# Optimization experiments

Hardware: AMD Instinct MI355X
Metric: run time of the kernel (lower is better)

Reference implementation:

```python
import jax, jax.numpy as jnp
import numpy as np

B, W, M = 16, 32, 512
NH, HALF, K, H = 64, 32, 8, 8
LK = W // 2               # long-conv kernel size
LOUT = W - 2 * (LK - 1)   # = 2 (dilated valid conv output length)
NSP = 10                  # n_spatial (hardcoded in module)
GC1_IN = (1 + LOUT) * K   # 24


def setup_inputs() -> dict:
    key = jax.random.key(0)
    ks = jax.random.split(key, 23)
    def n(k, shp, s=0.1):
        return jax.random.normal(k, shp, jnp.float32) * s
    return dict(
        x=jax.random.normal(ks[0], (B, W, M), jnp.float32),
        adj=jax.random.uniform(ks[1], (M, M), jnp.float32) / M,  # row-normalized-ish dense adj
        Wih=n(ks[2], (NH, 1)), Whh=n(ks[3], (NH, NH)),
        bih=n(ks[4], (NH,)), bhh=n(ks[5], (NH,)),
        W1=n(ks[6], (HALF, NH)), W2=n(ks[7], (HALF, NH)), b1=n(ks[8], (HALF,)),
        V=n(ks[9], (HALF,)), bv=n(ks[10], (1,)),
        Wb=n(ks[11], (M, M)), wb=n(ks[12], (1,)),
        conv_w=n(ks[13], (K, 1, W)), conv_b=n(ks[14], (K,)),
        convl_w=n(ks[15], (K, 1, LK)), convl_b=n(ks[16], (K,)),
        gc1_w=n(ks[17], (GC1_IN, NH)), gc1_b=n(ks[18], (NH,)),
        gc2_w=n(ks[19], (NH, NSP)), gc2_b=n(ks[20], (NSP,)),
        out_w=n(ks[21], (H, NSP + NH)), out_b=n(ks[22], (H,)),
    )


def reference(x, adj, Wih, Whh, bih, bhh, W1, W2, b1, V, bv, Wb, wb,
              conv_w, conv_b, convl_w, convl_b, gc1_w, gc1_b, gc2_w, gc2_b,
              out_w, out_b):
    b = x.shape[0]
    # [b, w, m] -> per-node sequences [b*m, w]
    seq = jnp.transpose(x, (0, 2, 1)).reshape(b * M, W)

    # vanilla tanh RNN, input_size=1 (batched over all b*m series)
    inp = seq[:, :, None] * Wih[:, 0] + (bih + bhh)          # [b*m, w, nh]
    def step(h, it):
        return jnp.tanh(it + h @ Whh.T), None
    h0 = jnp.zeros((b * M, NH), x.dtype)
    last_hid, _ = jax.lax.scan(step, h0, jnp.swapaxes(inp, 0, 1))
    last_hid = last_hid.reshape(b, M, NH)                    # out_temporal

    # pairwise additive attention: a[b,i,j] = V . elu(W1 h_j + W2 h_i + b1) + bv
    e1 = last_hid @ W1.T                                     # [b, m, half] (j role)
    e2 = last_hid @ W2.T                                     # [b, m, half] (i role)
    a = jax.nn.elu(e2[:, :, None, :] + e1[:, None, :, :] + b1)  # [b,m,m,half]
    a_mx = a @ V + bv                                        # [b, m, m]
    # F.normalize(p=2, dim=1)
    norm = jnp.sqrt(jnp.sum(a_mx * a_mx, axis=1, keepdims=True))
    a_mx = a_mx / jnp.maximum(norm, 1e-12)

    # per-node short conv (kernel == window -> out len 1) as a single matmul
    r_short = seq @ conv_w[:, 0, :].T + conv_b               # [b*m, k]
    # per-node dilated long conv, batched over all b*m series
    r_long = jax.lax.conv_general_dilated(
        seq[:, None, :], convl_w, window_strides=(1,), padding='VALID',
        rhs_dilation=(2,), dimension_numbers=('NCW', 'OIW', 'NCW'))
    r_long = r_long + convl_b[None, :, None]                 # [b*m, k, LOUT]
    r = jnp.concatenate([r_short[:, :, None], r_long], axis=-1)  # [b*m, k, 1+LOUT]
    r = jax.nn.relu(r.reshape(b, M, GC1_IN))

    # gated mix of static normalized adj and learned attention adj
    c = jax.nn.sigmoid(a_mx @ Wb + wb)
    adj_mix = adj[None] * c + a_mx * (1.0 - c)               # [b, m, m]

    # two dense graph conv layers: relu(adj @ (h @ W) + b)
    h1 = jax.nn.relu(adj_mix @ (r @ gc1_w) + gc1_b)          # [b, m, nh]
    out_spatial = jax.nn.relu(adj_mix @ (h1 @ gc2_w) + gc2_b)  # [b, m, nsp]

    feat = jnp.concatenate([out_spatial, last_hid], axis=-1)  # [b, m, nsp+nh]
    out = feat @ out_w.T + out_b                              # [b, m, h]
    return jnp.transpose(out, (0, 2, 1))                      # [b, h, m]
```

## Files before the change

kernel.cpp:

```cpp
#include <hip/hip_runtime.h>
#include <hip/hip_bf16.h>


typedef __attribute__((ext_vector_type(8))) short bf16x8;
typedef __attribute__((ext_vector_type(4))) float f32x4;
#define MFMA16 __builtin_amdgcn_mfma_f32_16x16x32_bf16

__device__ __forceinline__ unsigned short f2bf(float f) {
    unsigned u = __float_as_uint(f);
    u += 0x7fff + ((u >> 16) & 1);
    return (unsigned short)(u >> 16);
}
__device__ __forceinline__ float bf2f(unsigned short h) {
    return __uint_as_float(((unsigned)h) << 16);
}
__device__ __forceinline__ float fast_tanh(float x) {
    float e = __expf(2.f * x);
    return 1.f - 2.f / (e + 1.f);
}

__global__ __launch_bounds__(256) void wbt_kernel(
    const float* __restrict__ Wb, unsigned short* __restrict__ WbT)
{
    __shared__ float tile[32][33];
    int k0 = blockIdx.y * 32, n0 = blockIdx.x * 32;
    int t = threadIdx.x;
    for (int u = t; u < 1024; u += 256) {
        int r = u >> 5, c = u & 31;
        tile[r][c] = Wb[(k0 + r) * 512 + n0 + c];
    }
    __syncthreads();
    for (int u = t; u < 1024; u += 256) {
        int r = u >> 5, c = u & 31;
        WbT[(n0 + r) * 512 + k0 + c] = f2bf(tile[c][r]);
    }
}

__global__ __launch_bounds__(64) void rnn_kernel(
    const float* __restrict__ x, const float* __restrict__ Wih,
    const float* __restrict__ Whh, const float* __restrict__ bih,
    const float* __restrict__ bhh, float* __restrict__ lhT)
{
    int lane = threadIdx.x;
    int l15 = lane & 15, quad = lane >> 4;
    int row0 = blockIdx.x * 16;
    int b = row0 >> 9, m0 = row0 & 511;

    bf16x8 afr[4][2];
#pragma unroll
    for (int mt = 0; mt < 4; ++mt)
#pragma unroll
        for (int hf = 0; hf < 2; ++hf) {
            const float* src = Whh + (16 * mt + l15) * 64 + 32 * hf + quad * 8;
            union { bf16x8 v; unsigned short u[8]; } tmp;
#pragma unroll
            for (int j = 0; j < 8; ++j) tmp.u[j] = f2bf(src[j]);
            afr[mt][hf] = tmp.v;
        }
    float wihv[4][4], bsv[4][4];
#pragma unroll
    for (int mt = 0; mt < 4; ++mt)
#pragma unroll
        for (int r = 0; r < 4; ++r) {
            int n = 16 * mt + quad * 4 + r;
            wihv[mt][r] = Wih[n];
            bsv[mt][r]  = bih[n] + bhh[n];
        }

    __shared__ float xs[32][16];
    __shared__ __align__(16) unsigned short hs[16][72];
    for (int u = lane; u < 512; u += 64) {
        int t = u >> 4, mm = u & 15;
        xs[t][mm] = x[(b * 32 + t) * 512 + m0 + mm];
    }
    for (int u = lane; u < 16 * 72; u += 64) ((unsigned short*)hs)[u] = 0;
    __syncthreads();

    for (int t = 0; t < 32; ++t) {
        bf16x8 b0 = *(bf16x8*)(&hs[l15][quad * 8]);
        bf16x8 b1 = *(bf16x8*)(&hs[l15][32 + quad * 8]);
        float xt = xs[t][l15];
        f32x4 acc[4];
#pragma unroll
        for (int mt = 0; mt < 4; ++mt) {
            f32x4 z = {0.f, 0.f, 0.f, 0.f};
            acc[mt] = MFMA16(afr[mt][0], b0, z, 0, 0, 0);
            acc[mt] = MFMA16(afr[mt][1], b1, acc[mt], 0, 0, 0);
        }
#pragma unroll
        for (int mt = 0; mt < 4; ++mt) {
            ushort4 hw;
            float th[4];
#pragma unroll
            for (int r = 0; r < 4; ++r) {
                float v = acc[mt][r] + xt * wihv[mt][r] + bsv[mt][r];
                th[r] = fast_tanh(v);
            }
            hw.x = f2bf(th[0]); hw.y = f2bf(th[1]);
            hw.z = f2bf(th[2]); hw.w = f2bf(th[3]);
            *(ushort4*)(&hs[l15][16 * mt + quad * 4]) = hw;
            if (t == 31) {
#pragma unroll
                for (int r = 0; r < 4; ++r) {
                    int n = 16 * mt + quad * 4 + r;
                    lhT[n * 8192 + row0 + l15] = th[r];
                }
            }
        }
    }
}

__global__ __launch_bounds__(256) void e_kernel(
    const float* __restrict__ lhT, const float* __restrict__ W1,
    const float* __restrict__ W2, float* __restrict__ e1, float* __restrict__ e2)
{
    int wid  = threadIdx.x >> 6;
    int lane = threadIdx.x & 63;
    int row  = blockIdx.x * 4 + wid;
    int hh   = lane & 31;
    const float* Wm = (lane < 32) ? W1 : W2;
    float acc = 0.f;
#pragma unroll
    for (int n = 0; n < 64; ++n) acc += lhT[n * 8192 + row] * Wm[hh * 64 + n];
    float* dst = (lane < 32) ? e1 : e2;
    dst[row * 32 + hh] = acc;
}

__global__ __launch_bounds__(256) void amx_kernel(
    const float* __restrict__ e1, const float* __restrict__ e2,
    const float* __restrict__ b1p, const float* __restrict__ Vp,
    const float* __restrict__ bvp, float* __restrict__ amx,
    float* __restrict__ nrmss)
{
    int bb = blockIdx.z;
    int i0 = blockIdx.y * 64, j0 = blockIdx.x * 64;
    __shared__ float e2s[64][33], e1s[64][33];
    __shared__ float Vs[32];
    __shared__ float red[16][68];
    int t = threadIdx.x;
    for (int u = t; u < 2048; u += 256) {
        int r = u >> 5, c = u & 31;
        e2s[r][c] = e2[(bb * 512 + i0 + r) * 32 + c];
        e1s[r][c] = e1[(bb * 512 + j0 + r) * 32 + c] + b1p[c];
    }
    if (t < 32) Vs[t] = Vp[t];
    __syncthreads();
    int ti = (t >> 4) * 4, tj = (t & 15) * 4;
    float acc[4][4] = {};
#define ELUF(v) ((v) > 0.f ? (v) : (__expf(v) - 1.f))
#pragma unroll
    for (int h = 0; h < 32; ++h) {
        float vv = Vs[h];
        float xi[4], yj[4];
#pragma unroll
        for (int p = 0; p < 4; ++p) xi[p] = e2s[ti + p][h];
#pragma unroll
        for (int q = 0; q < 4; ++q) yj[q] = e1s[tj + q][h];
#pragma unroll
        for (int p = 0; p < 4; ++p)
#pragma unroll
            for (int q = 0; q < 4; ++q)
                acc[p][q] += vv * ELUF(xi[p] + yj[q]);
    }
    float bv = bvp[0];
    float ss[4] = {0.f, 0.f, 0.f, 0.f};
#pragma unroll
    for (int p = 0; p < 4; ++p) {
        float4 o;
        o.x = acc[p][0] + bv; o.y = acc[p][1] + bv;
        o.z = acc[p][2] + bv; o.w = acc[p][3] + bv;
        *(float4*)(amx + (bb * 512 + i0 + ti + p) * 512 + j0 + tj) = o;
        ss[0] += o.x * o.x; ss[1] += o.y * o.y;
        ss[2] += o.z * o.z; ss[3] += o.w * o.w;
    }
#pragma unroll
    for (int q = 0; q < 4; ++q) red[t >> 4][tj + q] = ss[q];
    __syncthreads();
    if (t < 64) {
        float s = 0.f;
#pragma unroll
        for (int g = 0; g < 16; ++g) s += red[g][t];
        atomicAdd(&nrmss[bb * 512 + j0 + t], s);
    }
}

__global__ void normfin_kernel(float* __restrict__ nrm)
{
    int j = blockIdx.x * 256 + threadIdx.x;
    nrm[j] = 1.f / fmaxf(sqrtf(nrm[j]), 1e-12f);
}

__global__ __launch_bounds__(256) void scale_kernel(
    const float* __restrict__ amx, const float* __restrict__ nrm,
    unsigned short* __restrict__ amxb)
{
    int idx = (blockIdx.x * 256 + threadIdx.x) * 4;
    int bb = idx >> 18;
    int j  = idx & 511;
    float4 v = *(const float4*)(amx + idx);
    const float* np = nrm + bb * 512 + j;
    ushort4 o;
    o.x = f2bf(v.x * np[0]); o.y = f2bf(v.y * np[1]);
    o.z = f2bf(v.z * np[2]); o.w = f2bf(v.w * np[3]);
    *(ushort4*)(amxb + idx) = o;
}

__global__ __launch_bounds__(256) void gemm_adjmix(
    const unsigned short* __restrict__ amxb, const unsigned short* __restrict__ WbT,
    const float* __restrict__ wbp, const float* __restrict__ adj,
    unsigned short* __restrict__ adjmix)
{
    int bb = blockIdx.z;
    int i0 = blockIdx.y * 64, j0 = blockIdx.x * 64;
    __shared__ __align__(16) short As[64 * 72];
    __shared__ __align__(16) short Bs[64 * 72];
    int t = threadIdx.x, w = t >> 6, lane = t & 63;
    int l15 = lane & 15, quad = lane >> 4;
    const unsigned short* Ag = amxb + bb * 262144;
    f32x4 acc[4] = {};
    for (int k0 = 0; k0 < 512; k0 += 64) {
        __syncthreads();
#pragma unroll
        for (int u0 = 0; u0 < 2; ++u0) {
            int u = t + u0 * 256;
            int i = u >> 3, o = u & 7;
            *(int4*)(As + i * 72 + o * 8) =
                *(const int4*)(Ag + (i0 + i) * 512 + k0 + o * 8);
            *(int4*)(Bs + i * 72 + o * 8) =
                *(const int4*)(WbT + (j0 + i) * 512 + k0 + o * 8);
        }
        __syncthreads();
        bf16x8 a0 = *(bf16x8*)(As + (16 * w + l15) * 72 + quad * 8);
        bf16x8 a1 = *(bf16x8*)(As + (16 * w + l15) * 72 + 32 + quad * 8);
#pragma unroll
        for (int nt = 0; nt < 4; ++nt) {
            bf16x8 b0 = *(bf16x8*)(Bs + (16 * nt + l15) * 72 + quad * 8);
            bf16x8 b1 = *(bf16x8*)(Bs + (16 * nt + l15) * 72 + 32 + quad * 8);
            acc[nt] = MFMA16(a0, b0, acc[nt], 0, 0, 0);
            acc[nt] = MFMA16(a1, b1, acc[nt], 0, 0, 0);
        }
    }
    float wb = wbp[0];
#pragma unroll
    for (int nt = 0; nt < 4; ++nt)
#pragma unroll
    for (int r = 0; r < 4; ++r) {
        int i = i0 + 16 * w + quad * 4 + r;
        int j = j0 + 16 * nt + l15;
        float s  = acc[nt][r] + wb;
        float cv = 1.f / (1.f + __expf(-s));
        float am = bf2f(Ag[i * 512 + j]);
        float ad = adj[i * 512 + j];
        adjmix[(bb * 512 + i) * 512 + j] = f2bf(ad * cv + am * (1.f - cv));
    }
}

__global__ void r_kernel(
    const float* __restrict__ x, const float* __restrict__ conv_w,
    const float* __restrict__ conv_b, const float* __restrict__ convl_w,
    const float* __restrict__ convl_b, float* __restrict__ rr)
{
    int idx = blockIdx.x * 256 + threadIdx.x;
    int k   = idx & 7;
    int row = idx >> 3;
    int bb  = row >> 9, m = row & 511;
    const float* xb = x + bb * 32 * 512 + m;
    float s = conv_b[k];
    for (int w = 0; w < 32; ++w) s += xb[w * 512] * conv_w[k * 32 + w];
    float l0 = convl_b[k], l1 = l0;
    for (int tt = 0; tt < 16; ++tt) {
        float wv = convl_w[k * 16 + tt];
        l0 += xb[(2 * tt) * 512] * wv;
        l1 += xb[(2 * tt + 1) * 512] * wv;
    }
    float* dst = rr + row * 24 + k * 3;
    dst[0] = fmaxf(s, 0.f);
    dst[1] = fmaxf(l0, 0.f);
    dst[2] = fmaxf(l1, 0.f);
}

__global__ void rg_kernel(const float* __restrict__ rr,
                          const float* __restrict__ gc1_w,
                          unsigned short* __restrict__ rgT)
{
    int idx = blockIdx.x * 256 + threadIdx.x;
    int m  = idx & 511;
    int n  = (idx >> 9) & 63;
    int bb = idx >> 15;
    const float* r = rr + (bb * 512 + m) * 24;
    float acc = 0.f;
#pragma unroll
    for (int c = 0; c < 24; ++c) acc += r[c] * gc1_w[c * 64 + n];
    rgT[idx] = f2bf(acc);
}

__global__ __launch_bounds__(256) void gemm_h1(
    const unsigned short* __restrict__ adjmix, const unsigned short* __restrict__ rgT,
    const float* __restrict__ gc1_b, float* __restrict__ h1)
{
    int bb = blockIdx.y;
    int i0 = blockIdx.x * 32;
    __shared__ __align__(16) short As[32 * 72];
    __shared__ __align__(16) short Bs[64 * 72];
    int t = threadIdx.x, w = t >> 6, lane = t & 63;
    int l15 = lane & 15, quad = lane >> 4;
    int rt = w & 1, ntb = (w >> 1) * 2;
    const unsigned short* Ag = adjmix + bb * 262144;
    const unsigned short* Bg = rgT + bb * 32768;
    f32x4 acc[2] = {};
    for (int k0 = 0; k0 < 512; k0 += 64) {
        __syncthreads();
        {
            int i = t >> 3, o = t & 7;
            *(int4*)(As + i * 72 + o * 8) =
                *(const int4*)(Ag + (i0 + i) * 512 + k0 + o * 8);
        }
#pragma unroll
        for (int u0 = 0; u0 < 2; ++u0) {
            int u = t + u0 * 256;
            int i = u >> 3, o = u & 7;
            *(int4*)(Bs + i * 72 + o * 8) =
                *(const int4*)(Bg + i * 512 + k0 + o * 8);
        }
        __syncthreads();
        bf16x8 a0 = *(bf16x8*)(As + (16 * rt + l15) * 72 + quad * 8);
        bf16x8 a1 = *(bf16x8*)(As + (16 * rt + l15) * 72 + 32 + quad * 8);
#pragma unroll
        for (int q = 0; q < 2; ++q) {
            int nt = ntb + q;
            bf16x8 b0 = *(bf16x8*)(Bs + (16 * nt + l15) * 72 + quad * 8);
            bf16x8 b1 = *(bf16x8*)(Bs + (16 * nt + l15) * 72 + 32 + quad * 8);
            acc[q] = MFMA16(a0, b0, acc[q], 0, 0, 0);
            acc[q] = MFMA16(a1, b1, acc[q], 0, 0, 0);
        }
    }
#pragma unroll
    for (int q = 0; q < 2; ++q)
#pragma unroll
    for (int r = 0; r < 4; ++r) {
        int i = i0 + 16 * rt + quad * 4 + r;
        int j = 16 * (ntb + q) + l15;
        h1[(bb * 512 + i) * 64 + j] = fmaxf(acc[q][r] + gc1_b[j], 0.f);
    }
}

__global__ void h1g_kernel(const float* __restrict__ h1,
                           const float* __restrict__ gc2_w, float* __restrict__ h1g)
{
    int idx = blockIdx.x * 256 + threadIdx.x;
    int row = idx / 10;
    int ns  = idx - row * 10;
    const float* hr = h1 + row * 64;
    float acc = 0.f;
#pragma unroll
    for (int n = 0; n < 64; ++n) acc += hr[n] * gc2_w[n * 10 + ns];
    h1g[idx] = acc;
}

__global__ __launch_bounds__(256) void osp_kernel(
    const unsigned short* __restrict__ adjmix, const float* __restrict__ h1g,
    const float* __restrict__ gc2_b, float* __restrict__ osp)
{
    int row0 = blockIdx.x * 4;
    int bb = row0 >> 9;
    int w = threadIdx.x >> 6, lane = threadIdx.x & 63;
    __shared__ float Bsm[10][512];
    for (int u = threadIdx.x; u < 5120; u += 256) {
        int k = u / 10, ns = u - k * 10;
        Bsm[ns][k] = h1g[bb * 5120 + u];
    }
    __syncthreads();
    int row = row0 + w;
    const unsigned short* Ar = adjmix + row * 512;
    float a[8];
#pragma unroll
    for (int q = 0; q < 8; ++q) a[q] = bf2f(Ar[lane + 64 * q]);
#pragma unroll
    for (int ns = 0; ns < 10; ++ns) {
        float s = 0.f;
#pragma unroll
        for (int q = 0; q < 8; ++q) s += a[q] * Bsm[ns][lane + 64 * q];
        for (int off = 32; off; off >>= 1) s += __shfl_down(s, off);
        if (lane == 0) osp[row * 10 + ns] = fmaxf(s + gc2_b[ns], 0.f);
    }
}

__global__ void out_kernel(
    const float* __restrict__ osp, const float* __restrict__ lhT,
    const float* __restrict__ out_w, const float* __restrict__ out_b,
    float* __restrict__ out)
{
    int idx = blockIdx.x * 256 + threadIdx.x;
    int m  = idx & 511;
    int hh = (idx >> 9) & 7;
    int bb = idx >> 12;
    const float* of = osp + (bb * 512 + m) * 10;
    float acc = out_b[hh];
#pragma unroll
    for (int n = 0; n < 10; ++n) acc += of[n] * out_w[hh * 74 + n];
#pragma unroll
    for (int n = 0; n < 64; ++n)
        acc += lhT[n * 8192 + bb * 512 + m] * out_w[hh * 74 + 10 + n];
    out[idx] = acc;
}

extern "C" void kernel_launch(void* const* d_in, const int* in_sizes, int n_in,
                              void* d_out, int out_size, void* d_ws, size_t ws_size,
                              hipStream_t stream)
{
    const float* x       = (const float*)d_in[0];
    const float* adj     = (const float*)d_in[1];
    const float* Wih     = (const float*)d_in[2];
    const float* Whh     = (const float*)d_in[3];
    const float* bih     = (const float*)d_in[4];
    const float* bhh     = (const float*)d_in[5];
    const float* W1      = (const float*)d_in[6];
    const float* W2      = (const float*)d_in[7];
    const float* b1      = (const float*)d_in[8];
    const float* V       = (const float*)d_in[9];
    const float* bv      = (const float*)d_in[10];
    const float* Wb      = (const float*)d_in[11];
    const float* wb      = (const float*)d_in[12];
    const float* conv_w  = (const float*)d_in[13];
    const float* conv_b  = (const float*)d_in[14];
    const float* convl_w = (const float*)d_in[15];
    const float* convl_b = (const float*)d_in[16];
    const float* gc1_w   = (const float*)d_in[17];
    const float* gc1_b   = (const float*)d_in[18];
    const float* gc2_w   = (const float*)d_in[19];
    const float* gc2_b   = (const float*)d_in[20];
    const float* out_w   = (const float*)d_in[21];
    const float* out_b   = (const float*)d_in[22];

    float* ws   = (float*)d_ws;
    float* lhT  = ws;
    float* e1   = lhT + 524288;
    float* e2   = e1 + 262144;
    float* amx  = e2 + 262144;
    float* nrm  = amx + 4194304;
    float* rr   = nrm + 8192;
    float* h1   = rr + 196608;
    float* h1g  = h1 + 524288;
    float* osp  = h1g + 81920;
    unsigned short* bfbase  = (unsigned short*)(osp + 81920);
    unsigned short* amxb    = bfbase;
    unsigned short* adjmixb = amxb + 4194304;
    unsigned short* WbT     = adjmixb + 4194304;
    unsigned short* rgT     = WbT + 262144;

    hipMemsetAsync(nrm, 0, 8192 * sizeof(float), stream);
    wbt_kernel<<<dim3(16, 16), 256, 0, stream>>>(Wb, WbT);
    rnn_kernel<<<512, 64, 0, stream>>>(x, Wih, Whh, bih, bhh, lhT);
    r_kernel<<<256, 256, 0, stream>>>(x, conv_w, conv_b, convl_w, convl_b, rr);
    e_kernel<<<2048, 256, 0, stream>>>(lhT, W1, W2, e1, e2);
    amx_kernel<<<dim3(8, 8, 16), 256, 0, stream>>>(e1, e2, b1, V, bv, amx, nrm);
    normfin_kernel<<<32, 256, 0, stream>>>(nrm);
    scale_kernel<<<4096, 256, 0, stream>>>(amx, nrm, amxb);
    gemm_adjmix<<<dim3(8, 8, 16), 256, 0, stream>>>(amxb, WbT, wb, adj, adjmixb);
    rg_kernel<<<2048, 256, 0, stream>>>(rr, gc1_w, rgT);
    gemm_h1<<<dim3(16, 16), 256, 0, stream>>>(adjmixb, rgT, gc1_b, h1);
    h1g_kernel<<<320, 256, 0, stream>>>(h1, gc2_w, h1g);
    osp_kernel<<<2048, 256, 0, stream>>>(adjmixb, h1g, gc2_b, osp);
    out_kernel<<<256, 256, 0, stream>>>(osp, lhT, out_w, out_b, (float*)d_out);
}
```

Baseline: 251.8 us.

## Fuse pipeline into six kernels, folding norm scaling into adjmix GEMM

Cuts the launch sequence from thirteen kernels plus a memset to six. Conv features, the gc1 projection, the Wb transpose and zeroing of the norm buffer are merged into one prep kernel. The e1/e2 projections are computed with MFMA inside the RNN kernel, and amx is stored directly as bf16. Column normalisation is applied while loading tiles in the adjmix GEMM, the gc2 projection moves into gemm_h1, and the osp and output stages are combined. This removes launches and fp32 intermediate round trips, but normalising after bf16 rounding adds a second rounding step and the GEMM does extra per-element conversion work.

```diff
diff --git a/kernel.cpp b/kernel.cpp
--- a/kernel.cpp
+++ b/kernel.cpp
@@ -1,5 +1,4 @@
 #include <hip/hip_runtime.h>
-#include <hip/hip_bf16.h>
 
 
 typedef __attribute__((ext_vector_type(8))) short bf16x8;
@@ -19,32 +18,74 @@
     return 1.f - 2.f / (e + 1.f);
 }
 
-__global__ __launch_bounds__(256) void wbt_kernel(
-    const float* __restrict__ Wb, unsigned short* __restrict__ WbT)
-{
-    __shared__ float tile[32][33];
-    int k0 = blockIdx.y * 32, n0 = blockIdx.x * 32;
-    int t = threadIdx.x;
-    for (int u = t; u < 1024; u += 256) {
-        int r = u >> 5, c = u & 31;
-        tile[r][c] = Wb[(k0 + r) * 512 + n0 + c];
-    }
-    __syncthreads();
-    for (int u = t; u < 1024; u += 256) {
-        int r = u >> 5, c = u & 31;
-        WbT[(n0 + r) * 512 + k0 + c] = f2bf(tile[c][r]);
-    }
-}
-
-__global__ __launch_bounds__(64) void rnn_kernel(
+__global__ __launch_bounds__(256) void prep_kernel(
+    const float* __restrict__ x, const float* __restrict__ conv_w,
+    const float* __restrict__ conv_b, const float* __restrict__ convl_w,
+    const float* __restrict__ convl_b, const float* __restrict__ gc1_w,
+    unsigned short* __restrict__ rgT,
+    const float* __restrict__ Wb, unsigned short* __restrict__ WbT,
+    float* __restrict__ nrmss)
+{
+    int blk = blockIdx.x, t = threadIdx.x;
+    if (blk < 256) {
+        int r0 = blk * 32;
+        int bb = r0 >> 9, m0 = r0 & 511;
+        __shared__ float rrs[32][25];
+        {
+            int k = t & 7, rl = t >> 3;
+            const float* xb = x + bb * 16384 + m0 + rl;
+            float s = conv_b[k];
+            for (int w = 0; w < 32; ++w) s += xb[w * 512] * conv_w[k * 32 + w];
+            float l0 = convl_b[k], l1 = l0;
+            for (int tt = 0; tt < 16; ++tt) {
+                float wv = convl_w[k * 16 + tt];
+                l0 += xb[(2 * tt) * 512] * wv;
+                l1 += xb[(2 * tt + 1) * 512] * wv;
+            }
+            rrs[rl][k * 3 + 0] = fmaxf(s, 0.f);
+            rrs[rl][k * 3 + 1] = fmaxf(l0, 0.f);
+            rrs[rl][k * 3 + 2] = fmaxf(l1, 0.f);
+        }
+        __syncthreads();
+        int rl = t & 31, nb = t >> 5;
+#pragma unroll
+        for (int q = 0; q < 8; ++q) {
+            int n = nb * 8 + q;
+            float acc = 0.f;
+#pragma unroll
+            for (int c = 0; c < 24; ++c) acc += rrs[rl][c] * gc1_w[c * 64 + n];
+            rgT[bb * 32768 + n * 512 + m0 + rl] = f2bf(acc);
+        }
+    } else if (blk < 512) {
+        int bid = blk - 256;
+        int nb = (bid & 15) * 32, kb = (bid >> 4) * 32;
+        __shared__ float tile[32][33];
+        for (int u = t; u < 1024; u += 256) {
+            int r = u >> 5, c = u & 31;
+            tile[r][c] = Wb[(kb + r) * 512 + nb + c];
+        }
+        __syncthreads();
+        for (int u = t; u < 1024; u += 256) {
+            int r = u >> 5, c = u & 31;
+            WbT[(nb + r) * 512 + kb + c] = f2bf(tile[c][r]);
+        }
+    } else {
+        nrmss[(blk - 512) * 256 + t] = 0.f;
+    }
+}
+
+__global__ __launch_bounds__(256) void rnn_kernel(
     const float* __restrict__ x, const float* __restrict__ Wih,
     const float* __restrict__ Whh, const float* __restrict__ bih,
-    const float* __restrict__ bhh, float* __restrict__ lhT)
-{
-    int lane = threadIdx.x;
+    const float* __restrict__ bhh, const float* __restrict__ W1,
+    const float* __restrict__ W2, float* __restrict__ lh,
+    float* __restrict__ e1, float* __restrict__ e2)
+{
+    int t = threadIdx.x, wid = t >> 6, lane = t & 63;
     int l15 = lane & 15, quad = lane >> 4;
-    int row0 = blockIdx.x * 16;
-    int b = row0 >> 9, m0 = row0 & 511;
+    int rowblk = blockIdx.x * 64;
+    int row0 = rowblk + wid * 16;
+    int b = rowblk >> 9, mb = rowblk & 511;
 
     bf16x8 afr[4][2];
 #pragma unroll
@@ -57,6 +98,20 @@
             for (int j = 0; j < 8; ++j) tmp.u[j] = f2bf(src[j]);
             afr[mt][hf] = tmp.v;
         }
+    bf16x8 wfr[2][2][2];
+#pragma unroll
+    for (int e = 0; e < 2; ++e)
+#pragma unroll
+        for (int nt = 0; nt < 2; ++nt)
+#pragma unroll
+            for (int kf = 0; kf < 2; ++kf) {
+                const float* Wsrc = (e ? W2 : W1);
+                const float* src = Wsrc + (16 * nt + l15) * 64 + 32 * kf + quad * 8;
+                union { bf16x8 v; unsigned short u[8]; } tmp;
+#pragma unroll
+                for (int j = 0; j < 8; ++j) tmp.u[j] = f2bf(src[j]);
+                wfr[e][nt][kf] = tmp.v;
+            }
     float wihv[4][4], bsv[4][4];
 #pragma unroll
     for (int mt = 0; mt < 4; ++mt)
@@ -67,19 +122,21 @@
             bsv[mt][r]  = bih[n] + bhh[n];
         }
 
-    __shared__ float xs[32][16];
-    __shared__ __align__(16) unsigned short hs[16][72];
-    for (int u = lane; u < 512; u += 64) {
-        int t = u >> 4, mm = u & 15;
-        xs[t][mm] = x[(b * 32 + t) * 512 + m0 + mm];
-    }
-    for (int u = lane; u < 16 * 72; u += 64) ((unsigned short*)hs)[u] = 0;
+    __shared__ float xs[32][64];
+    __shared__ __align__(16) unsigned short hs[4][16][72];
+    for (int u = t; u < 2048; u += 256) {
+        int tt = u >> 6, c = u & 63;
+        xs[tt][c] = x[(b * 32 + tt) * 512 + mb + c];
+    }
+    for (int u = lane; u < 16 * 72; u += 64) (&hs[wid][0][0])[u] = 0;
     __syncthreads();
 
-    for (int t = 0; t < 32; ++t) {
-        bf16x8 b0 = *(bf16x8*)(&hs[l15][quad * 8]);
-        bf16x8 b1 = *(bf16x8*)(&hs[l15][32 + quad * 8]);
-        float xt = xs[t][l15];
+    int mloc = wid * 16;
+    float th[4][4];
+    for (int tstep = 0; tstep < 32; ++tstep) {
+        bf16x8 b0 = *(bf16x8*)(&hs[wid][l15][quad * 8]);
+        bf16x8 b1 = *(bf16x8*)(&hs[wid][l15][32 + quad * 8]);
+        float xt = xs[tstep][mloc + l15];
         f32x4 acc[4];
 #pragma unroll
         for (int mt = 0; mt < 4; ++mt) {
@@ -90,46 +147,40 @@
 #pragma unroll
         for (int mt = 0; mt < 4; ++mt) {
             ushort4 hw;
-            float th[4];
-#pragma unroll
-            for (int r = 0; r < 4; ++r) {
-                float v = acc[mt][r] + xt * wihv[mt][r] + bsv[mt][r];
-                th[r] = fast_tanh(v);
-            }
-            hw.x = f2bf(th[0]); hw.y = f2bf(th[1]);
-            hw.z = f2bf(th[2]); hw.w = f2bf(th[3]);
-            *(ushort4*)(&hs[l15][16 * mt + quad * 4]) = hw;
-            if (t == 31) {
-#pragma unroll
-                for (int r = 0; r < 4; ++r) {
-                    int n = 16 * mt + quad * 4 + r;
-                    lhT[n * 8192 + row0 + l15] = th[r];
-                }
-            }
-        }
-    }
-}
-
-__global__ __launch_bounds__(256) void e_kernel(
-    const float* __restrict__ lhT, const float* __restrict__ W1,
-    const float* __restrict__ W2, float* __restrict__ e1, float* __restrict__ e2)
-{
-    int wid  = threadIdx.x >> 6;
-    int lane = threadIdx.x & 63;
-    int row  = blockIdx.x * 4 + wid;
-    int hh   = lane & 31;
-    const float* Wm = (lane < 32) ? W1 : W2;
-    float acc = 0.f;
-#pragma unroll
-    for (int n = 0; n < 64; ++n) acc += lhT[n * 8192 + row] * Wm[hh * 64 + n];
-    float* dst = (lane < 32) ? e1 : e2;
-    dst[row * 32 + hh] = acc;
+#pragma unroll
+            for (int r = 0; r < 4; ++r)
+                th[mt][r] = fast_tanh(acc[mt][r] + xt * wihv[mt][r] + bsv[mt][r]);
+            hw.x = f2bf(th[mt][0]); hw.y = f2bf(th[mt][1]);
+            hw.z = f2bf(th[mt][2]); hw.w = f2bf(th[mt][3]);
+            *(ushort4*)(&hs[wid][l15][16 * mt + quad * 4]) = hw;
+        }
+    }
+#pragma unroll
+    for (int mt = 0; mt < 4; ++mt)
+        *(float4*)(lh + (row0 + l15) * 64 + 16 * mt + quad * 4) =
+            make_float4(th[mt][0], th[mt][1], th[mt][2], th[mt][3]);
+
+    bf16x8 a0 = *(bf16x8*)(&hs[wid][l15][quad * 8]);
+    bf16x8 a1 = *(bf16x8*)(&hs[wid][l15][32 + quad * 8]);
+#pragma unroll
+    for (int e = 0; e < 2; ++e) {
+        float* dst = e ? e2 : e1;
+#pragma unroll
+        for (int nt = 0; nt < 2; ++nt) {
+            f32x4 z = {0.f, 0.f, 0.f, 0.f};
+            f32x4 ee = MFMA16(a0, wfr[e][nt][0], z, 0, 0, 0);
+            ee = MFMA16(a1, wfr[e][nt][1], ee, 0, 0, 0);
+#pragma unroll
+            for (int r = 0; r < 4; ++r)
+                dst[(row0 + quad * 4 + r) * 32 + 16 * nt + l15] = ee[r];
+        }
+    }
 }
 
 __global__ __launch_bounds__(256) void amx_kernel(
     const float* __restrict__ e1, const float* __restrict__ e2,
     const float* __restrict__ b1p, const float* __restrict__ Vp,
-    const float* __restrict__ bvp, float* __restrict__ amx,
+    const float* __restrict__ bvp, unsigned short* __restrict__ amxb,
     float* __restrict__ nrmss)
 {
     int bb = blockIdx.z;
@@ -166,12 +217,12 @@
     float ss[4] = {0.f, 0.f, 0.f, 0.f};
 #pragma unroll
     for (int p = 0; p < 4; ++p) {
-        float4 o;
-        o.x = acc[p][0] + bv; o.y = acc[p][1] + bv;
-        o.z = acc[p][2] + bv; o.w = acc[p][3] + bv;
-        *(float4*)(amx + (bb * 512 + i0 + ti + p) * 512 + j0 + tj) = o;
-        ss[0] += o.x * o.x; ss[1] += o.y * o.y;
-        ss[2] += o.z * o.z; ss[3] += o.w * o.w;
+        float v0 = acc[p][0] + bv, v1 = acc[p][1] + bv;
+        float v2 = acc[p][2] + bv, v3 = acc[p][3] + bv;
+        ushort4 o;
+        o.x = f2bf(v0); o.y = f2bf(v1); o.z = f2bf(v2); o.w = f2bf(v3);
+        *(ushort4*)(amxb + (bb * 512 + i0 + ti + p) * 512 + j0 + tj) = o;
+        ss[0] += v0 * v0; ss[1] += v1 * v1; ss[2] += v2 * v2; ss[3] += v3 * v3;
     }
 #pragma unroll
     for (int q = 0; q < 4; ++q) red[t >> 4][tj + q] = ss[q];
@@ -184,38 +235,20 @@
     }
 }
 
-__global__ void normfin_kernel(float* __restrict__ nrm)
-{
-    int j = blockIdx.x * 256 + threadIdx.x;
-    nrm[j] = 1.f / fmaxf(sqrtf(nrm[j]), 1e-12f);
-}
-
-__global__ __launch_bounds__(256) void scale_kernel(
-    const float* __restrict__ amx, const float* __restrict__ nrm,
-    unsigned short* __restrict__ amxb)
-{
-    int idx = (blockIdx.x * 256 + threadIdx.x) * 4;
-    int bb = idx >> 18;
-    int j  = idx & 511;
-    float4 v = *(const float4*)(amx + idx);
-    const float* np = nrm + bb * 512 + j;
-    ushort4 o;
-    o.x = f2bf(v.x * np[0]); o.y = f2bf(v.y * np[1]);
-    o.z = f2bf(v.z * np[2]); o.w = f2bf(v.w * np[3]);
-    *(ushort4*)(amxb + idx) = o;
-}
-
 __global__ __launch_bounds__(256) void gemm_adjmix(
     const unsigned short* __restrict__ amxb, const unsigned short* __restrict__ WbT,
     const float* __restrict__ wbp, const float* __restrict__ adj,
-    unsigned short* __restrict__ adjmix)
+    const float* __restrict__ nrmss, unsigned short* __restrict__ adjmix)
 {
     int bb = blockIdx.z;
     int i0 = blockIdx.y * 64, j0 = blockIdx.x * 64;
     __shared__ __align__(16) short As[64 * 72];
     __shared__ __align__(16) short Bs[64 * 72];
+    __shared__ float rn[512];
     int t = threadIdx.x, w = t >> 6, lane = t & 63;
     int l15 = lane & 15, quad = lane >> 4;
+    for (int u = t; u < 512; u += 256)
+        rn[u] = 1.f / fmaxf(sqrtf(nrmss[bb * 512 + u]), 1e-12f);
     const unsigned short* Ag = amxb + bb * 262144;
     f32x4 acc[4] = {};
     for (int k0 = 0; k0 < 512; k0 += 64) {
@@ -224,10 +257,15 @@
         for (int u0 = 0; u0 < 2; ++u0) {
             int u = t + u0 * 256;
             int i = u >> 3, o = u & 7;
-            *(int4*)(As + i * 72 + o * 8) =
-                *(const int4*)(Ag + (i0 + i) * 512 + k0 + o * 8);
             *(int4*)(Bs + i * 72 + o * 8) =
                 *(const int4*)(WbT + (j0 + i) * 512 + k0 + o * 8);
+            union { int4 v; unsigned short us[8]; } ur;
+            ur.v = *(const int4*)(Ag + (i0 + i) * 512 + k0 + o * 8);
+            union { int4 v; unsigned short us[8]; } ow;
+#pragma unroll
+            for (int c = 0; c < 8; ++c)
+                ow.us[c] = f2bf(bf2f(ur.us[c]) * rn[k0 + o * 8 + c]);
+            *(int4*)(As + i * 72 + o * 8) = ow.v;
         }
         __syncthreads();
         bf16x8 a0 = *(bf16x8*)(As + (16 * w + l15) * 72 + quad * 8);
@@ -249,59 +287,22 @@
         int j = j0 + 16 * nt + l15;
         float s  = acc[nt][r] + wb;
         float cv = 1.f / (1.f + __expf(-s));
-        float am = bf2f(Ag[i * 512 + j]);
+        float am = bf2f(Ag[i * 512 + j]) * rn[j];
         float ad = adj[i * 512 + j];
         adjmix[(bb * 512 + i) * 512 + j] = f2bf(ad * cv + am * (1.f - cv));
     }
 }
 
-__global__ void r_kernel(
-    const float* __restrict__ x, const float* __restrict__ conv_w,
-    const float* __restrict__ conv_b, const float* __restrict__ convl_w,
-    const float* __restrict__ convl_b, float* __restrict__ rr)
-{
-    int idx = blockIdx.x * 256 + threadIdx.x;
-    int k   = idx & 7;
-    int row = idx >> 3;
-    int bb  = row >> 9, m = row & 511;
-    const float* xb = x + bb * 32 * 512 + m;
-    float s = conv_b[k];
-    for (int w = 0; w < 32; ++w) s += xb[w * 512] * conv_w[k * 32 + w];
-    float l0 = convl_b[k], l1 = l0;
-    for (int tt = 0; tt < 16; ++tt) {
-        float wv = convl_w[k * 16 + tt];
-        l0 += xb[(2 * tt) * 512] * wv;
-        l1 += xb[(2 * tt + 1) * 512] * wv;
-    }
-    float* dst = rr + row * 24 + k * 3;
-    dst[0] = fmaxf(s, 0.f);
-    dst[1] = fmaxf(l0, 0.f);
-    dst[2] = fmaxf(l1, 0.f);
-}
-
-__global__ void rg_kernel(const float* __restrict__ rr,
-                          const float* __restrict__ gc1_w,
-                          unsigned short* __restrict__ rgT)
-{
-    int idx = blockIdx.x * 256 + threadIdx.x;
-    int m  = idx & 511;
-    int n  = (idx >> 9) & 63;
-    int bb = idx >> 15;
-    const float* r = rr + (bb * 512 + m) * 24;
-    float acc = 0.f;
-#pragma unroll
-    for (int c = 0; c < 24; ++c) acc += r[c] * gc1_w[c * 64 + n];
-    rgT[idx] = f2bf(acc);
-}
-
 __global__ __launch_bounds__(256) void gemm_h1(
     const unsigned short* __restrict__ adjmix, const unsigned short* __restrict__ rgT,
-    const float* __restrict__ gc1_b, float* __restrict__ h1)
+    const float* __restrict__ gc1_b, const float* __restrict__ gc2_w,
+    float* __restrict__ h1g)
 {
     int bb = blockIdx.y;
     int i0 = blockIdx.x * 32;
     __shared__ __align__(16) short As[32 * 72];
     __shared__ __align__(16) short Bs[64 * 72];
+    __shared__ float h1s[32][72];
     int t = threadIdx.x, w = t >> 6, lane = t & 63;
     int l15 = lane & 15, quad = lane >> 4;
     int rt = w & 1, ntb = (w >> 1) * 2;
@@ -338,70 +339,71 @@
     for (int q = 0; q < 2; ++q)
 #pragma unroll
     for (int r = 0; r < 4; ++r) {
-        int i = i0 + 16 * rt + quad * 4 + r;
+        int il = 16 * rt + quad * 4 + r;
         int j = 16 * (ntb + q) + l15;
-        h1[(bb * 512 + i) * 64 + j] = fmaxf(acc[q][r] + gc1_b[j], 0.f);
-    }
-}
-
-__global__ void h1g_kernel(const float* __restrict__ h1,
-                           const float* __restrict__ gc2_w, float* __restrict__ h1g)
-{
-    int idx = blockIdx.x * 256 + threadIdx.x;
-    int row = idx / 10;
-    int ns  = idx - row * 10;
-    const float* hr = h1 + row * 64;
-    float acc = 0.f;
-#pragma unroll
-    for (int n = 0; n < 64; ++n) acc += hr[n] * gc2_w[n * 10 + ns];
-    h1g[idx] = acc;
-}
-
-__global__ __launch_bounds__(256) void osp_kernel(
+        h1s[il][j] = fmaxf(acc[q][r] + gc1_b[j], 0.f);
+    }
+    __syncthreads();
+    for (int u = t; u < 320; u += 256) {
+        int row = u / 10, ns = u - row * 10;
+        float a2 = 0.f;
+#pragma unroll
+        for (int j = 0; j < 64; ++j) a2 += h1s[row][j] * gc2_w[j * 10 + ns];
+        h1g[(bb * 512 + i0 + row) * 10 + ns] = a2;
+    }
+}
+
+__global__ __launch_bounds__(256) void ospout_kernel(
     const unsigned short* __restrict__ adjmix, const float* __restrict__ h1g,
-    const float* __restrict__ gc2_b, float* __restrict__ osp)
-{
-    int row0 = blockIdx.x * 4;
-    int bb = row0 >> 9;
-    int w = threadIdx.x >> 6, lane = threadIdx.x & 63;
+    const float* __restrict__ gc2_b, const float* __restrict__ lh,
+    const float* __restrict__ out_w, const float* __restrict__ out_b,
+    float* __restrict__ out)
+{
+    int r0 = blockIdx.x * 4;
+    int bb = r0 >> 9;
+    int wid = threadIdx.x >> 6, lane = threadIdx.x & 63;
     __shared__ float Bsm[10][512];
+    __shared__ float ow[8][80];
+    __shared__ float ob[8], g2b[10];
     for (int u = threadIdx.x; u < 5120; u += 256) {
         int k = u / 10, ns = u - k * 10;
         Bsm[ns][k] = h1g[bb * 5120 + u];
     }
+    if (threadIdx.x < 8)  ob[threadIdx.x]  = out_b[threadIdx.x];
+    if (threadIdx.x < 10) g2b[threadIdx.x] = gc2_b[threadIdx.x];
+    for (int u = threadIdx.x; u < 592; u += 256) {
+        int hh = u / 74, c = u - hh * 74;
+        ow[hh][c] = out_w[u];
+    }
     __syncthreads();
-    int row = row0 + w;
+    int row = r0 + wid, m = row & 511;
     const unsigned short* Ar = adjmix + row * 512;
     float a[8];
 #pragma unroll
     for (int q = 0; q < 8; ++q) a[q] = bf2f(Ar[lane + 64 * q]);
+    float os[10];
 #pragma unroll
     for (int ns = 0; ns < 10; ++ns) {
         float s = 0.f;
 #pragma unroll
         for (int q = 0; q < 8; ++q) s += a[q] * Bsm[ns][lane + 64 * q];
-        for (int off = 32; off; off >>= 1) s += __shfl_down(s, off);
-        if (lane == 0) osp[row * 10 + ns] = fmaxf(s + gc2_b[ns], 0.f);
-    }
-}
-
-__global__ void out_kernel(
-    const float* __restrict__ osp, const float* __restrict__ lhT,
-    const float* __restrict__ out_w, const float* __restrict__ out_b,
-    float* __restrict__ out)
-{
-    int idx = blockIdx.x * 256 + threadIdx.x;
-    int m  = idx & 511;
-    int hh = (idx >> 9) & 7;
-    int bb = idx >> 12;
-    const float* of = osp + (bb * 512 + m) * 10;
-    float acc = out_b[hh];
-#pragma unroll
-    for (int n = 0; n < 10; ++n) acc += of[n] * out_w[hh * 74 + n];
-#pragma unroll
-    for (int n = 0; n < 64; ++n)
-        acc += lhT[n * 8192 + bb * 512 + m] * out_w[hh * 74 + 10 + n];
-    out[idx] = acc;
+#pragma unroll
+        for (int off = 32; off; off >>= 1) s += __shfl_xor(s, off);
+        os[ns] = fmaxf(s + g2b[ns], 0.f);
+    }
+    float lv = lh[row * 64 + lane];
+#pragma unroll
+    for (int hh = 0; hh < 8; ++hh) {
+        float t1 = lv * ow[hh][10 + lane];
+#pragma unroll
+        for (int off = 32; off; off >>= 1) t1 += __shfl_xor(t1, off);
+        if (lane == hh) {
+            float acc = ob[hh] + t1;
+#pragma unroll
+            for (int ns = 0; ns < 10; ++ns) acc += os[ns] * ow[hh][ns];
+            out[bb * 4096 + hh * 512 + m] = acc;
+        }
+    }
 }
 
 extern "C" void kernel_launch(void* const* d_in, const int* in_sizes, int n_in,
@@ -432,34 +434,26 @@
     const float* out_w   = (const float*)d_in[21];
     const float* out_b   = (const float*)d_in[22];
 
-    float* ws   = (float*)d_ws;
-    float* lhT  = ws;
-    float* e1   = lhT + 524288;
-    float* e2   = e1 + 262144;
-    float* amx  = e2 + 262144;
-    float* nrm  = amx + 4194304;
-    float* rr   = nrm + 8192;
-    float* h1   = rr + 196608;
-    float* h1g  = h1 + 524288;
-    float* osp  = h1g + 81920;
-    unsigned short* bfbase  = (unsigned short*)(osp + 81920);
-    unsigned short* amxb    = bfbase;
+    float* ws    = (float*)d_ws;
+    float* lh    = ws;
+    float* e1    = lh + 524288;
+    float* e2    = e1 + 262144;
+    float* nrmss = e2 + 262144;
+    float* h1g   = nrmss + 8192;
+    unsigned short* amxb    = (unsigned short*)(h1g + 81920);
     unsigned short* adjmixb = amxb + 4194304;
     unsigned short* WbT     = adjmixb + 4194304;
     unsigned short* rgT     = WbT + 262144;
 
-    hipMemsetAsync(nrm, 0, 8192 * sizeof(float), stream);
-    wbt_kernel<<<dim3(16, 16), 256, 0, stream>>>(Wb, WbT);
-    rnn_kernel<<<512, 64, 0, stream>>>(x, Wih, Whh, bih, bhh, lhT);
-    r_kernel<<<256, 256, 0, stream>>>(x, conv_w, conv_b, convl_w, convl_b, rr);
-    e_kernel<<<2048, 256, 0, stream>>>(lhT, W1, W2, e1, e2);
-    amx_kernel<<<dim3(8, 8, 16), 256, 0, stream>>>(e1, e2, b1, V, bv, amx, nrm);
-    normfin_kernel<<<32, 256, 0, stream>>>(nrm);
-    scale_kernel<<<4096, 256, 0, stream>>>(amx, nrm, amxb);
-    gemm_adjmix<<<dim3(8, 8, 16), 256, 0, stream>>>(amxb, WbT, wb, adj, adjmixb);
-    rg_kernel<<<2048, 256, 0, stream>>>(rr, gc1_w, rgT);
-    gemm_h1<<<dim3(16, 16), 256, 0, stream>>>(adjmixb, rgT, gc1_b, h1);
-    h1g_kernel<<<320, 256, 0, stream>>>(h1, gc2_w, h1g);
-    osp_kernel<<<2048, 256, 0, stream>>>(adjmixb, h1g, gc2_b, osp);
-    out_kernel<<<256, 256, 0, stream>>>(osp, lhT, out_w, out_b, (float*)d_out);
-}
+    prep_kernel<<<544, 256, 0, stream>>>(x, conv_w, conv_b, convl_w, convl_b,
+                                         gc1_w, rgT, Wb, WbT, nrmss);
+    rnn_kernel<<<128, 256, 0, stream>>>(x, Wih, Whh, bih, bhh, W1, W2,
+                                        lh, e1, e2);
+    amx_kernel<<<dim3(8, 8, 16), 256, 0, stream>>>(e1, e2, b1, V, bv,
+                                                   amxb, nrmss);
+    gemm_adjmix<<<dim3(8, 8, 16), 256, 0, stream>>>(amxb, WbT, wb, adj,
+                                                    nrmss, adjmixb);
+    gemm_h1<<<dim3(16, 16), 256, 0, stream>>>(adjmixb, rgT, gc1_b, gc2_w, h1g);
+    ospout_kernel<<<2048, 256, 0, stream>>>(adjmixb, h1g, gc2_b, lh,
+                                            out_w, out_b, (float*)d_out);
+}
```

Measured after the change: 220.3 us. 12.5% less time.
